# Kernel optimization log

Hardware: AMD Instinct MI355X
Metric: run time of the kernel (lower is better)

Reference implementation:

```python
import jax, jax.numpy as jnp
import numpy as np

B = 1024      # jets per batch
P = 150       # TOTAL_PARTICLES per jet
N = B * P     # total nodes
DEG = 16      # avg degree
E = N * DEG
H = 256       # GNN_HIDDEN_DIM
K = 6         # GNN_K
NC = 10       # NUM_CLUSTERS
IN = 3


def setup_inputs() -> dict:
    key = jax.random.key(0)
    ks = jax.random.split(key, 16)
    x = jax.random.normal(ks[0], (N, IN), jnp.float32)
    # kNN-like within-jet edges: each node sends to DEG random nodes of its own jet
    src = jnp.repeat(jnp.arange(N, dtype=jnp.int32), DEG)
    tgt = (src // P) * P + jax.random.randint(ks[1], (E,), 0, P, dtype=jnp.int32)
    edge_index = jnp.stack([src, tgt])  # [2, E]
    batch = jnp.arange(N, dtype=jnp.int32) // P  # sorted graph ids, exactly P per graph
    inp = dict(x=x, edge_index=edge_index, batch=batch)
    dims = [(IN, H), (H, H), (H, H), (H, H)]
    for i, (di, do) in enumerate(dims):
        s = 1.0 / np.sqrt(di)
        inp[f"W{i+1}"] = jax.random.uniform(ks[2 + i], (K, di, do), jnp.float32, -s, s)
        inp[f"b{i+1}"] = jnp.zeros((do,), jnp.float32)
    for i in range(3):
        inp[f"g{i+1}"] = jnp.ones((H,), jnp.float32)
        inp[f"be{i+1}"] = jnp.zeros((H,), jnp.float32)
    inp["centers"] = jax.random.normal(ks[10], (NC, 2), jnp.float32) * 0.2
    inp["log_temp"] = jnp.float32(2.0)
    return inp


def _lap_weights(src, tgt, n):
    # PyG ChebConv norm with lambda_max=2, sym normalization, self-loops removed:
    # scaled Laplacian L_hat = -D^{-1/2} A D^{-1/2} (zero diagonal)
    w = (src != tgt).astype(jnp.float32)          # remove self-loops
    deg = jax.ops.segment_sum(w, src, num_segments=n)
    dis = jnp.where(deg > 0, 1.0 / jnp.sqrt(deg), 0.0)
    return -(dis[src] * w * dis[tgt])             # [E]


def _cheb(x, W, b, src, tgt, lw, n):
    # Chebyshev recurrence: T0=x, T1=Lx, Tk=2L T_{k-1} - T_{k-2}
    prop = lambda h: jax.ops.segment_sum(lw[:, None] * h[src], tgt, num_segments=n)
    Tx0 = x
    out = Tx0 @ W[0]
    Tx1 = prop(Tx0)
    out = out + Tx1 @ W[1]
    for k in range(2, W.shape[0]):
        Tx2 = 2.0 * prop(Tx1) - Tx0
        out = out + Tx2 @ W[k]
        Tx0, Tx1 = Tx1, Tx2
    return out + b


def _bn(h, g, b):
    # BatchNorm1d, training-mode batch statistics (biased var), eps=1e-5
    m = h.mean(0)
    v = h.var(0)
    return (h - m) * jax.lax.rsqrt(v + 1e-5) * g + b


def reference(x, edge_index, batch, W1, b1, W2, b2, W3, b3, W4, b4,
              g1, be1, g2, be2, g3, be3, centers, log_temp):
    n = x.shape[0]
    src, tgt = edge_index[0], edge_index[1]
    lw = _lap_weights(src, tgt, n)
    lrelu = lambda h: jax.nn.leaky_relu(h, 0.01)
    h = lrelu(_bn(_cheb(x, W1, b1, src, tgt, lw, n), g1, be1))
    h = lrelu(_bn(_cheb(h, W2, b2, src, tgt, lw, n), g2, be2))
    h = lrelu(_bn(_cheb(h, W3, b3, src, tgt, lw, n), g3, be3))
    h = _cheb(h, W4, b4, src, tgt, lw, n)
    h = h / jnp.maximum(jnp.linalg.norm(h, axis=1, keepdims=True), 1e-12)  # F.normalize
    # to_dense_batch: batch is sorted with exactly P nodes per graph -> pure reshape,
    # node_mask is all True
    dense_h = h.reshape(B, P, -1)          # [B, P, H]
    dense_c = x[:, :2].reshape(B, P, 2)    # (eta, phi)
    dist = ((dense_c[:, :, None, :] - centers) ** 2).sum(-1)   # [B, P, NC]
    T = jnp.exp(jnp.clip(log_temp, -2.0, 3.0))
    assignment = jax.nn.softmax(-T * dist, axis=-1)            # mask is all-true
    pooled = jnp.einsum('bnk,bnd->bkd', assignment, dense_h)   # [B, NC, H]
    pooled = pooled / (assignment.sum(1)[:, :, None] + 1e-8)
    return pooled.reshape(B, -1)  # [B, NC*H]
```

## Files before the change

### kernel.cpp

```cpp
#include <hip/hip_runtime.h>
#include <cstdio>

#define NODES 153600
#define PJ 150
#define NJETS 1024
#define DEG 16
#define NEDGE (NODES*DEG)
#define HD 256
#define NCL 10

#define LSTR 192
#define TNS  64

typedef unsigned short u16;
typedef _Float16 f16;
typedef f16 f16x8 __attribute__((ext_vector_type(8)));
typedef u16 u16x8 __attribute__((ext_vector_type(8)));
typedef u16 u16x4 __attribute__((ext_vector_type(4)));
typedef float f32x4 __attribute__((ext_vector_type(4)));

__device__ inline float h2f(u16 u) { union { u16 s; f16 h; } v; v.s = u; return (float)v.h; }
__device__ inline u16 f2h(float f) { union { u16 s; f16 h; } v; v.h = (f16)f; return v.s; }
__device__ inline int swz(int seg, int key) { return (seg & ~7) | ((seg & 7) ^ (key & 7)); }

__global__ void k_diag(float* out, float code) {
  if (blockIdx.x == 0 && threadIdx.x == 0) out[0] = code;
}


__global__ __launch_bounds__(256) void k_discounts(const int* __restrict__ tgt,
                                                   int* __restrict__ counts,
                                                   float* __restrict__ dis) {
  int i = blockIdx.x*256 + threadIdx.x;
  if (i < NEDGE) atomicAdd(&counts[tgt[i]], 1);
  if (i < NODES) {
    int cnt = 0;
#pragma unroll
    for (int j = 0; j < DEG; ++j) cnt += (tgt[i*DEG + j] != i) ? 1 : 0;
    dis[i] = (cnt > 0) ? rsqrtf((float)cnt) : 0.f;
  }
}

__global__ __launch_bounds__(256) void k_scan(const int* __restrict__ counts, int* __restrict__ rowptr, int* __restrict__ cursor) {
  int j = blockIdx.x*256 + threadIdx.x;
  if (j >= NJETS) return;
  int run = j*PJ*DEG;
  for (int l = 0; l < PJ; ++l) {
    int idx = j*PJ + l;
    int cnt = counts[idx];
    rowptr[idx] = run;
    cursor[idx] = run;
    run += cnt;
  }
  if (j == 0) rowptr[NODES] = NEDGE;
}

__global__ __launch_bounds__(256) void k_fill(const int* __restrict__ src_, const int* __restrict__ tgt_,
                                              const float* __restrict__ dis, int* __restrict__ cursor,
                                              unsigned char* __restrict__ ccol, float* __restrict__ cw) {
  int e = blockIdx.x*256 + threadIdx.x;
  if (e >= NEDGE) return;
  int s = src_[e], t = tgt_[e];
  int pos = atomicAdd(&cursor[t], 1);
  ccol[pos] = (unsigned char)(s % PJ);
  cw[pos] = (s != t) ? -(dis[s]*dis[t]) : 0.f;
}

__global__ __launch_bounds__(256) void k_prepW(const float* __restrict__ Wa, const float* __restrict__ Wb,
                                               const float* __restrict__ Wc, u16* __restrict__ WT,
                                               float* __restrict__ stats ,
                                               float* __restrict__ rn) {
  int i = blockIdx.x*256 + threadIdx.x;
  if (i < 3*256*1536) {
    int layer = i / (256*1536);
    int rem = i - layer*(256*1536);
    int cout = rem / 1536, k = rem - cout*1536;
    int term = k >> 8, cin = k & 255;
    const float* W = (layer == 0) ? Wa : (layer == 1) ? Wb : Wc;
    WT[i] = f2h(W[(size_t)term*65536 + cin*256 + cout]);
  }
  if (i < 3*2*HD) stats[i] = 0.f;
  if (i < NODES) rn[i] = 0.f;
}

__global__ __launch_bounds__(512) void k_l1(const float* __restrict__ x,
                                            const int* __restrict__ rowptr,
                                            const unsigned char* __restrict__ ccol,
                                            const float* __restrict__ cw,
                                            const float* __restrict__ W1,
                                            const float* __restrict__ b1,
                                            float* __restrict__ stats,
                                            u16* __restrict__ outc) {
  __shared__ float Ta[450], Tb[450];
  __shared__ float Tall_s[PJ*18];
  __shared__ float wl[18*256];
  __shared__ float cw_s[PJ*DEG];
  __shared__ u16  col_s[PJ*DEG];
  __shared__ int  rp_s[PJ+1];
  int j = blockIdx.x, tid = threadIdx.x;
  int jb = j*PJ, e0 = jb*DEG;
  for (int i = tid; i < 18*256; i += 512) wl[i] = W1[i];
  for (int i = tid; i < PJ*DEG; i += 512) { cw_s[i] = cw[e0+i]; col_s[i] = (u16)ccol[e0+i]; }
  for (int i = tid; i < PJ+1; i += 512) rp_s[i] = rowptr[jb+i] - e0;
  if (tid < 450) Ta[tid] = x[(size_t)jb*3 + tid];
  __syncthreads();
  int r = tid/3, c = tid - r*3;
  float* cur = Ta; float* oth = Tb;
  if (tid < 450) Tall_s[r*18 + c] = cur[tid];
  for (int t = 1; t < 6; ++t) {
    if (tid < 450) {
      int es = rp_s[r], ee = rp_s[r+1];
      float acc = 0.f;
      for (int e = es; e < ee; ++e) acc += cw_s[e]*cur[(int)col_s[e]*3 + c];
      float v = (t == 1) ? acc : 2.f*acc - oth[tid];
      oth[tid] = v;
      Tall_s[r*18 + t*3 + c] = v;
    }
    __syncthreads();
    float* tmp = cur; cur = oth; oth = tmp;
  }
  int cc = tid & 255, rhalf = tid >> 8;
  float bc = b1[cc];
  float s = 0.f, s2 = 0.f;
  int r0 = rhalf*75;
  for (int rr = r0; rr < r0 + 75; ++rr) {
    float acc = 0.f;
#pragma unroll
    for (int i = 0; i < 18; ++i) acc += Tall_s[rr*18 + i] * wl[i*256 + cc];
    outc[(size_t)(jb+rr)*HD + cc] = f2h(acc);
    float vb = acc + bc;
    s += vb; s2 += vb*vb;
  }
  atomicAdd(&stats[cc], s);
  atomicAdd(&stats[HD + cc], s2);
}

template<int OMODE>
__global__ __launch_bounds__(1024, 4) void k_cheb(const u16* __restrict__ IN,
                                                  const u16* __restrict__ WTu,
                                                  const int* __restrict__ rowptr,
                                                  const unsigned char* __restrict__ ccol,
                                                  const float* __restrict__ cw,
                                                  const float* __restrict__ statsPrev,
                                                  const float* __restrict__ gP,
                                                  const float* __restrict__ beP,
                                                  const float* __restrict__ bP,
                                                  const float* __restrict__ bCur,
                                                  float* __restrict__ statsCur,
                                                  float* __restrict__ rn,
                                                  u16* __restrict__ OUTp) {
  __shared__ u16 Ls[160*LSTR];
  __shared__ u16 Tn[2][160*TNS];
  __shared__ u16 Tt[2][64*LSTR];
  __shared__ float bnA[HD], bnB[HD];
  int j = blockIdx.x, tid = threadIdx.x;
  int jb = j*PJ;
  int lane = tid & 63, wid = tid >> 6;
  int wm = wid >> 3, wn = wid & 7;
  int lr = lane & 15, lg = lane >> 4;
  int ph = wn >> 2, cs = wn & 3;
  int cown = cs*16 + lr;
  int key   = lr & 7;
  int segA0 = ((lg    ) ^ key) * 8;
  int segA1 = ((lg + 4) ^ key) * 8;
  int pOff[5] = { segA0, segA1, 64 + segA0, 64 + segA1, 128 + segA0 };
  int ep0 = ((cown >> 3) ^ ((lg & 1)*4 + 0)) * 8 + (cown & 7);
  int ep1 = ((cown >> 3) ^ ((lg & 1)*4 + 1)) * 8 + (cown & 7);
  int ep2 = ((cown >> 3) ^ ((lg & 1)*4 + 2)) * 8 + (cown & 7);
  int ep3 = ((cown >> 3) ^ ((lg & 1)*4 + 3)) * 8 + (cown & 7);
  int cownL = cown * LSTR;
  const f16* WT = (const f16*)WTu;
  const f16* wtb = WT + (size_t)(wn*32 + lr)*1536 + lg*8;

  if (tid < HD) {
    const float invN = 1.f/(float)NODES;
    float m = statsPrev[tid]*invN;
    float var = statsPrev[HD+tid]*invN - m*m;
    float A = rsqrtf(var + 1e-5f) * gP[tid];
    bnA[tid] = A;
    bnB[tid] = (bP[tid] - m)*A + beP[tid];
  }
  {
    u16x8 z = {0,0,0,0,0,0,0,0};
    for (int i = tid; i < 3840; i += 1024) *(u16x8*)&Ls[i*8] = z;
    for (int i = tid; i < 160; i += 1024) {
      int h = i >= 80 ? 1 : 0;
      int rem = i - h*80;
      int row = 150 + (rem >> 3), seg = rem & 7;
      *(u16x8*)&Tn[h][row*TNS + seg*8] = z;
    }
  }
  __syncthreads();
  if (tid < PJ) {
    int es = rowptr[jb + tid], ee = rowptr[jb + tid + 1];
    for (int e = es; e < ee; ++e) {
      int c = (int)ccol[e];
      int a = tid*LSTR + swz(c >> 3, tid)*8 + (c & 7);
      Ls[a] = f2h(h2f(Ls[a]) + 2.f*cw[e]);
    }
  }
  f32x4 acc[5][2];
#pragma unroll
  for (int a = 0; a < 5; ++a)
#pragma unroll
    for (int b = 0; b < 2; ++b) acc[a][b] = (f32x4)0.f;

  u16x4 tc0, tc1, tc2, tc3, tc4, tp0, tp1, tp2, tp3, tp4;

  for (int qp = 0; qp < 2; ++qp) {
    __syncthreads();
    for (int i = tid; i < 2400; i += 1024) {
      int h = (i >= 1200) ? 1 : 0;
      int rem = i - h*1200;
      int row = rem >> 3, seg = rem & 7;
      int c0 = (qp*2+h)*64 + seg*8;
      u16x8 v = *(const u16x8*)&IN[(size_t)(jb+row)*HD + c0];
      u16x8 o;
#pragma unroll
      for (int u = 0; u < 8; ++u) {
        float f = h2f(v[u])*bnA[c0+u] + bnB[c0+u];
        o[u] = f2h((f > 0.f) ? f : 0.01f*f);
      }
      *(u16x8*)&Tn[h][row*TNS + (seg ^ (row & 7))*8] = o;
    }
    __syncthreads();
    for (int i = tid; i < 2560; i += 1024) {
      int h = (i >= 1280) ? 1 : 0;
      int rem = i - h*1280;
      int c = rem & 63, m = rem >> 6;
      u16x8 v;
#pragma unroll
      for (int u = 0; u < 8; ++u) {
        int r = m*8 + u;
        v[u] = Tn[h][r*TNS + ((c >> 3) ^ (r & 7))*8 + (c & 7)];
      }
      *(u16x8*)&Tt[h][c*LSTR + swz(m, c)*8] = v;
    }
#define TINIT(MF, TC, TP) { int r0 = wm*80 + MF*16 + lg*4; u16x4 t; \
    t[0] = Tn[ph][(r0+0)*TNS + ep0]; t[1] = Tn[ph][(r0+1)*TNS + ep1]; \
    t[2] = Tn[ph][(r0+2)*TNS + ep2]; t[3] = Tn[ph][(r0+3)*TNS + ep3]; \
    TC = t; TP = t; }
    TINIT(0, tc0, tp0) TINIT(1, tc1, tp1) TINIT(2, tc2, tp2) TINIT(3, tc3, tp3) TINIT(4, tc4, tp4)
#undef TINIT
    __syncthreads();
#pragma unroll 1
    for (int t = 0; t < 6; ++t) {
#pragma unroll
      for (int h = 0; h < 2; ++h) {
        int kbase = t*256 + (qp*2+h)*64;
#pragma unroll
        for (int ks = 0; ks < 64; ks += 32) {
          int segA = (ks == 0) ? segA0 : segA1;
          f16x8 a[5], bv[2];
#pragma unroll
          for (int nf = 0; nf < 2; ++nf)
            bv[nf] = *(const f16x8*)&wtb[nf*24576 + kbase + ks];
#pragma unroll
          for (int mf = 0; mf < 5; ++mf) {
            int row = wm*80 + mf*16 + lr;
            a[mf] = *(const f16x8*)&Tn[h][row*TNS + segA];
          }
          __builtin_amdgcn_s_setprio(1);
#pragma unroll
          for (int nf = 0; nf < 2; ++nf)
#pragma unroll
            for (int mf = 0; mf < 5; ++mf)
              acc[mf][nf] = __builtin_amdgcn_mfma_f32_16x16x32_f16(a[mf], bv[nf], acc[mf][nf], 0, 0, 0);
          __builtin_amdgcn_s_setprio(0);
        }
      }
      if (t < 5) {
        f32x4 pacc[5];
#pragma unroll
        for (int mf = 0; mf < 5; ++mf) pacc[mf] = (f32x4)0.f;
#pragma unroll
        for (int ks = 0; ks < 5; ++ks) {
          f16x8 b = *(const f16x8*)&Tt[ph][cownL + pOff[ks]];
          __builtin_amdgcn_s_setprio(1);
#pragma unroll
          for (int mf = 0; mf < 5; ++mf) {
            int row = wm*80 + mf*16 + lr;
            f16x8 a = *(const f16x8*)&Ls[row*LSTR + pOff[ks]];
            pacc[mf] = __builtin_amdgcn_mfma_f32_16x16x32_f16(a, b, pacc[mf], 0, 0, 0);
          }
          __builtin_amdgcn_s_setprio(0);
        }
        __syncthreads();
#define TEPI(MF, TC, TP) { int r0 = wm*80 + MF*16 + lg*4; u16x4 o; \
        { float v0_ = (t == 0) ? 0.5f*pacc[MF][0] : pacc[MF][0] - h2f(TP[0]); o[0] = f2h(v0_); } \
        { float v1_ = (t == 0) ? 0.5f*pacc[MF][1] : pacc[MF][1] - h2f(TP[1]); o[1] = f2h(v1_); } \
        { float v2_ = (t == 0) ? 0.5f*pacc[MF][2] : pacc[MF][2] - h2f(TP[2]); o[2] = f2h(v2_); } \
        { float v3_ = (t == 0) ? 0.5f*pacc[MF][3] : pacc[MF][3] - h2f(TP[3]); o[3] = f2h(v3_); } \
        Tn[ph][(r0+0)*TNS + ep0] = o[0]; Tn[ph][(r0+1)*TNS + ep1] = o[1]; \
        Tn[ph][(r0+2)*TNS + ep2] = o[2]; Tn[ph][(r0+3)*TNS + ep3] = o[3]; \
        int sgT = wm*10 + MF*2 + (lg >> 1); \
        int segT = (sgT & ~7) | ((sgT & 7) ^ key); \
        *(u16x4*)&Tt[ph][cownL + segT*8 + (lg & 1)*4] = o; \
        TP = TC; TC = o; }
        TEPI(0, tc0, tp0) TEPI(1, tc1, tp1) TEPI(2, tc2, tp2) TEPI(3, tc3, tp3) TEPI(4, tc4, tp4)
#undef TEPI
        __syncthreads();
      }
    }
  }
  if (OMODE == 0) {
#pragma unroll
    for (int nf = 0; nf < 2; ++nf) {
      int col = wn*32 + nf*16 + lr;
      float bc = bCur[col];
      float s = 0.f, s2 = 0.f;
#pragma unroll
      for (int mf = 0; mf < 5; ++mf) {
        int row = wm*80 + mf*16 + lg*4;
#pragma unroll
        for (int e = 0; e < 4; ++e) {
          int r = row + e;
          if (r < PJ) {
            float v = acc[mf][nf][e];
            OUTp[(size_t)(jb+r)*HD + col] = f2h(v);
            float vb = v + bc;
            s += vb; s2 += vb*vb;
          }
        }
      }
      s  += __shfl_xor(s, 16, 64);  s  += __shfl_xor(s, 32, 64);
      s2 += __shfl_xor(s2, 16, 64); s2 += __shfl_xor(s2, 32, 64);
      if (lg == 0) {
        atomicAdd(&statsCur[col], s);
        atomicAdd(&statsCur[HD + col], s2);
      }
    }
  } else {
    float bc[2];
#pragma unroll
    for (int nf = 0; nf < 2; ++nf) bc[nf] = bCur[wn*32 + nf*16 + lr];
#pragma unroll
    for (int mf = 0; mf < 5; ++mf) {
      int row = wm*80 + mf*16 + lg*4;
#pragma unroll
      for (int e = 0; e < 4; ++e) {
        int r = row + e;
        float srow = 0.f;
        if (r < PJ) {
#pragma unroll
          for (int nf = 0; nf < 2; ++nf) {
            int col = wn*32 + nf*16 + lr;
            float v = acc[mf][nf][e];
            OUTp[(size_t)(jb+r)*HD + col] = f2h(v);
            float vb = v + bc[nf];
            srow += vb*vb;
          }
        }
        srow += __shfl_xor(srow, 1, 64);
        srow += __shfl_xor(srow, 2, 64);
        srow += __shfl_xor(srow, 4, 64);
        srow += __shfl_xor(srow, 8, 64);
        if (lr == 0 && r < PJ) atomicAdd(&rn[jb + r], srow);
      }
    }
  }
}


__global__ __launch_bounds__(256) void k_pool(const u16* __restrict__ h, const float* __restrict__ rn,
                                              const float* __restrict__ bias, const float* __restrict__ x,
                                              const float* __restrict__ centers, const float* __restrict__ log_temp,
                                              float* __restrict__ out) {
  __shared__ float a_s[PJ][NCL];
  __shared__ float colsum[NCL];
  __shared__ float inv_s[PJ];
  int j = blockIdx.x;
  int tid = threadIdx.x;
  float T = expf(fminf(fmaxf(log_temp[0], -2.f), 3.f));
  if (tid < PJ) {
    int g = j*PJ + tid;
    inv_s[tid] = 1.f / fmaxf(sqrtf(rn[g]), 1e-12f);
    float eta = x[(size_t)g*3], phi = x[(size_t)g*3 + 1];
    float d[NCL];
    float dmin = 1e30f;
#pragma unroll
    for (int k = 0; k < NCL; ++k) {
      float dx = eta - centers[2*k], dy = phi - centers[2*k+1];
      d[k] = dx*dx + dy*dy;
      dmin = fminf(dmin, d[k]);
    }
    float s = 0.f, ek[NCL];
#pragma unroll
    for (int k = 0; k < NCL; ++k) { ek[k] = expf(-T*(d[k]-dmin)); s += ek[k]; }
    float invs = 1.f/s;
#pragma unroll
    for (int k = 0; k < NCL; ++k) a_s[tid][k] = ek[k]*invs;
  }
  __syncthreads();
  if (tid < NCL) {
    float s = 0.f;
    for (int n = 0; n < PJ; ++n) s += a_s[n][tid];
    colsum[tid] = s;
  }
  __syncthreads();
  int c = tid;
  float bc = bias[c];
  float acc[NCL] = {};
  for (int n = 0; n < PJ; ++n) {
    float hv = (h2f(h[(size_t)(j*PJ + n)*HD + c]) + bc) * inv_s[n];
#pragma unroll
    for (int k = 0; k < NCL; ++k) acc[k] += a_s[n][k]*hv;
  }
#pragma unroll
  for (int k = 0; k < NCL; ++k)
    out[(size_t)j*(NCL*HD) + k*HD + c] = acc[k] / (colsum[k] + 1e-8f);
}


extern "C" void kernel_launch(void* const* d_in, const int* in_sizes, int n_in,
                              void* d_out, int out_size, void* d_ws, size_t ws_size,
                              hipStream_t stream) {
  (void)in_sizes; (void)n_in; (void)out_size;
  const float* x   = (const float*)d_in[0];
  const int*   ei  = (const int*)d_in[1];
  const int*   srcA = ei;
  const int*   tgtA = ei + NEDGE;
  const float* W1  = (const float*)d_in[3];
  const float* b1  = (const float*)d_in[4];
  const float* W2  = (const float*)d_in[5];
  const float* b2  = (const float*)d_in[6];
  const float* W3  = (const float*)d_in[7];
  const float* b3  = (const float*)d_in[8];
  const float* W4  = (const float*)d_in[9];
  const float* b4  = (const float*)d_in[10];
  const float* g1  = (const float*)d_in[11];
  const float* be1 = (const float*)d_in[12];
  const float* g2  = (const float*)d_in[13];
  const float* be2 = (const float*)d_in[14];
  const float* g3  = (const float*)d_in[15];
  const float* be3 = (const float*)d_in[16];
  const float* centers  = (const float*)d_in[17];
  const float* log_temp = (const float*)d_in[18];
  float* out = (float*)d_out;

  auto rb = [](size_t b) { return (b + 255) & ~(size_t)255; };
  size_t need = 2*rb((size_t)NODES*HD*2)
              + rb((size_t)3*256*1536*2)
              + 3*rb((size_t)NODES*4)
              + rb((size_t)(NODES+1)*4)
              + rb((size_t)NEDGE)
              + rb((size_t)NEDGE*4)
              + rb((size_t)3*2*HD*4)
              + rb((size_t)NODES*4);
  fprintf(stderr, "[kernel_launch] ws_size=%zu need=%zu\n", ws_size, need);
  if (d_ws == nullptr || ws_size < need) {
    float code = 1.0e6f + (float)(ws_size >> 20);
    k_diag<<<1, 1, 0, stream>>>(out, code);
    return;
  }

  char* wp = (char*)d_ws;
  auto alloc = [&](size_t b) -> void* {
    void* p = (void*)wp;
    wp += (b + 255) & ~(size_t)255;
    return p;
  };
  u16*   OUTA = (u16*)alloc((size_t)NODES*HD*2);
  u16*   OUTB = (u16*)alloc((size_t)NODES*HD*2);
  u16*   Wcat = (u16*)alloc((size_t)3*256*1536*2);
  float* dis  = (float*)alloc((size_t)NODES*4);
  int*   counts = (int*)alloc((size_t)NODES*4);
  int*   cursor = (int*)alloc((size_t)NODES*4);
  int*   rowptr = (int*)alloc((size_t)(NODES+1)*4);
  unsigned char* ccol = (unsigned char*)alloc((size_t)NEDGE);
  float* cw     = (float*)alloc((size_t)NEDGE*4);
  float* stats  = (float*)alloc((size_t)3*2*HD*4);
  float* rn     = (float*)alloc((size_t)NODES*4);
  float* s0 = stats, *s1 = stats + 512, *s2 = stats + 1024;

  hipMemsetAsync(counts, 0, (size_t)NODES*4, stream);
  k_discounts<<<(NEDGE+255)/256, 256, 0, stream>>>(tgtA, counts, dis);
  k_scan<<<(NJETS+255)/256, 256, 0, stream>>>(counts, rowptr, cursor);
  k_fill<<<(NEDGE+255)/256, 256, 0, stream>>>(srcA, tgtA, dis, cursor, ccol, cw);

  k_prepW<<<(3*256*1536+255)/256, 256, 0, stream>>>(W2, W3, W4, Wcat, stats, rn);

  k_l1<<<NJETS, 512, 0, stream>>>(x, rowptr, ccol, cw, W1, b1, s0, OUTA);

  k_cheb<0><<<NJETS, 1024, 0, stream>>>(OUTA, Wcat,            rowptr, ccol, cw, s0, g1, be1, b1, b2, s1, rn, OUTB);
  k_cheb<0><<<NJETS, 1024, 0, stream>>>(OUTB, Wcat + 393216,   rowptr, ccol, cw, s1, g2, be2, b2, b3, s2, rn, OUTA);
  k_cheb<1><<<NJETS, 1024, 0, stream>>>(OUTA, Wcat + 2*393216, rowptr, ccol, cw, s2, g3, be3, b3, b4, s2, rn, OUTB);

  k_pool<<<NJETS, 256, 0, stream>>>(OUTB, rn, b4, x, centers, log_temp, out);
}
```

Baseline: 1.256 ms.

## Fuse normalization and soft-cluster pooling into final Chebyshev layer epilogue

The last Chebyshev layer now computes per-row L2 norms in shared memory, builds the softmax cluster assignments, and accumulates pooled outputs directly from the accumulator registers. The separate pooling kernel, the global row-norm buffer with its atomics, and the half-precision store of the final features are removed. This saves a launch plus a full write and read of the last hidden layer, and uses full-precision values for pooling. In exchange the epilogue adds several block barriers, shared-memory atomics and register pressure to an already heavy kernel.

```diff
diff --git a/kernel.cpp b/kernel.cpp
--- a/kernel.cpp
+++ b/kernel.cpp
@@ -68,8 +68,7 @@
 
 __global__ __launch_bounds__(256) void k_prepW(const float* __restrict__ Wa, const float* __restrict__ Wb,
                                                const float* __restrict__ Wc, u16* __restrict__ WT,
-                                               float* __restrict__ stats ,
-                                               float* __restrict__ rn) {
+                                               float* __restrict__ stats ) {
   int i = blockIdx.x*256 + threadIdx.x;
   if (i < 3*256*1536) {
     int layer = i / (256*1536);
@@ -80,7 +79,6 @@
     WT[i] = f2h(W[(size_t)term*65536 + cin*256 + cout]);
   }
   if (i < 3*2*HD) stats[i] = 0.f;
-  if (i < NODES) rn[i] = 0.f;
 }
 
 __global__ __launch_bounds__(512) void k_l1(const float* __restrict__ x,
@@ -147,7 +145,10 @@
                                                   const float* __restrict__ bP,
                                                   const float* __restrict__ bCur,
                                                   float* __restrict__ statsCur,
-                                                  float* __restrict__ rn,
+                                                  const float* __restrict__ x,
+                                                  const float* __restrict__ centers,
+                                                  const float* __restrict__ log_temp,
+                                                  float* __restrict__ outF,
                                                   u16* __restrict__ OUTp) {
   __shared__ u16 Ls[160*LSTR];
   __shared__ u16 Tn[2][160*TNS];
@@ -331,84 +332,93 @@
       }
     }
   } else {
-    float bc[2];
-#pragma unroll
-    for (int nf = 0; nf < 2; ++nf) bc[nf] = bCur[wn*32 + nf*16 + lr];
+    __syncthreads();
+    float* aS    = (float*)Ls;
+    float* colS  = aS + PJ*NCL;
+    float* rnS   = colS + 16;
+    float* poolS = rnS + 160;
+    for (int i = tid; i < 160 + NCL*256; i += 1024) {
+      if (i < 160) rnS[i] = 0.f; else poolS[i-160] = 0.f;
+    }
+    if (tid < PJ) {
+      int g = jb + tid;
+      float T = expf(fminf(fmaxf(log_temp[0], -2.f), 3.f));
+      float eta = x[(size_t)g*3], phi = x[(size_t)g*3 + 1];
+      float d[NCL]; float dmin = 1e30f;
+#pragma unroll
+      for (int k = 0; k < NCL; ++k) {
+        float dx = eta - centers[2*k], dy = phi - centers[2*k+1];
+        d[k] = dx*dx + dy*dy; dmin = fminf(dmin, d[k]);
+      }
+      float s = 0.f, ek[NCL];
+#pragma unroll
+      for (int k = 0; k < NCL; ++k) { ek[k] = expf(-T*(d[k]-dmin)); s += ek[k]; }
+      float invs = 1.f/s;
+#pragma unroll
+      for (int k = 0; k < NCL; ++k) aS[tid*NCL + k] = ek[k]*invs;
+    }
+    __syncthreads();
+    if (tid < NCL) {
+      float s = 0.f;
+      for (int n = 0; n < PJ; ++n) s += aS[n*NCL + tid];
+      colS[tid] = s;
+    }
+    float bc0 = bCur[wn*32 + lr], bc1 = bCur[wn*32 + 16 + lr];
 #pragma unroll
     for (int mf = 0; mf < 5; ++mf) {
       int row = wm*80 + mf*16 + lg*4;
 #pragma unroll
       for (int e = 0; e < 4; ++e) {
         int r = row + e;
-        float srow = 0.f;
-        if (r < PJ) {
-#pragma unroll
-          for (int nf = 0; nf < 2; ++nf) {
-            int col = wn*32 + nf*16 + lr;
-            float v = acc[mf][nf][e];
-            OUTp[(size_t)(jb+r)*HD + col] = f2h(v);
-            float vb = v + bc[nf];
-            srow += vb*vb;
-          }
-        }
+        float v0 = acc[mf][0][e] + bc0, v1 = acc[mf][1][e] + bc1;
+        float srow = v0*v0 + v1*v1;
         srow += __shfl_xor(srow, 1, 64);
         srow += __shfl_xor(srow, 2, 64);
         srow += __shfl_xor(srow, 4, 64);
         srow += __shfl_xor(srow, 8, 64);
-        if (lr == 0 && r < PJ) atomicAdd(&rn[jb + r], srow);
-      }
-    }
-  }
-}
-
-
-__global__ __launch_bounds__(256) void k_pool(const u16* __restrict__ h, const float* __restrict__ rn,
-                                              const float* __restrict__ bias, const float* __restrict__ x,
-                                              const float* __restrict__ centers, const float* __restrict__ log_temp,
-                                              float* __restrict__ out) {
-  __shared__ float a_s[PJ][NCL];
-  __shared__ float colsum[NCL];
-  __shared__ float inv_s[PJ];
-  int j = blockIdx.x;
-  int tid = threadIdx.x;
-  float T = expf(fminf(fmaxf(log_temp[0], -2.f), 3.f));
-  if (tid < PJ) {
-    int g = j*PJ + tid;
-    inv_s[tid] = 1.f / fmaxf(sqrtf(rn[g]), 1e-12f);
-    float eta = x[(size_t)g*3], phi = x[(size_t)g*3 + 1];
-    float d[NCL];
-    float dmin = 1e30f;
+        if (lr == 0 && r < PJ) atomicAdd(&rnS[r], srow);
+      }
+    }
+    __syncthreads();
+    if (tid < PJ) rnS[tid] = 1.f / fmaxf(sqrtf(rnS[tid]), 1e-12f);
+    __syncthreads();
+    float part0[NCL], part1[NCL];
+#pragma unroll
+    for (int k = 0; k < NCL; ++k) { part0[k] = 0.f; part1[k] = 0.f; }
+#pragma unroll
+    for (int mf = 0; mf < 5; ++mf) {
+      int row = wm*80 + mf*16 + lg*4;
+#pragma unroll
+      for (int e = 0; e < 4; ++e) {
+        int r = row + e;
+        if (r < PJ) {
+          float inv = rnS[r];
+          float h0 = (acc[mf][0][e] + bc0)*inv;
+          float h1 = (acc[mf][1][e] + bc1)*inv;
+#pragma unroll
+          for (int k = 0; k < NCL; ++k) {
+            float a = aS[r*NCL + k];
+            part0[k] += a*h0; part1[k] += a*h1;
+          }
+        }
+      }
+    }
 #pragma unroll
     for (int k = 0; k < NCL; ++k) {
-      float dx = eta - centers[2*k], dy = phi - centers[2*k+1];
-      d[k] = dx*dx + dy*dy;
-      dmin = fminf(dmin, d[k]);
-    }
-    float s = 0.f, ek[NCL];
-#pragma unroll
-    for (int k = 0; k < NCL; ++k) { ek[k] = expf(-T*(d[k]-dmin)); s += ek[k]; }
-    float invs = 1.f/s;
-#pragma unroll
-    for (int k = 0; k < NCL; ++k) a_s[tid][k] = ek[k]*invs;
-  }
-  __syncthreads();
-  if (tid < NCL) {
-    float s = 0.f;
-    for (int n = 0; n < PJ; ++n) s += a_s[n][tid];
-    colsum[tid] = s;
-  }
-  __syncthreads();
-  int c = tid;
-  float bc = bias[c];
-  float acc[NCL] = {};
-  for (int n = 0; n < PJ; ++n) {
-    float hv = (h2f(h[(size_t)(j*PJ + n)*HD + c]) + bc) * inv_s[n];
-#pragma unroll
-    for (int k = 0; k < NCL; ++k) acc[k] += a_s[n][k]*hv;
-  }
-#pragma unroll
-  for (int k = 0; k < NCL; ++k)
-    out[(size_t)j*(NCL*HD) + k*HD + c] = acc[k] / (colsum[k] + 1e-8f);
+      float p0 = part0[k], p1 = part1[k];
+      p0 += __shfl_xor(p0, 16, 64); p0 += __shfl_xor(p0, 32, 64);
+      p1 += __shfl_xor(p1, 16, 64); p1 += __shfl_xor(p1, 32, 64);
+      if (lg == 0) {
+        atomicAdd(&poolS[k*256 + wn*32 + lr], p0);
+        atomicAdd(&poolS[k*256 + wn*32 + 16 + lr], p1);
+      }
+    }
+    __syncthreads();
+    for (int i = tid; i < NCL*256; i += 1024) {
+      int k = i >> 8;
+      outF[(size_t)j*(NCL*HD) + i] = poolS[i] / (colS[k] + 1e-8f);
+    }
+  }
 }
 
 
@@ -445,8 +455,7 @@
               + rb((size_t)(NODES+1)*4)
               + rb((size_t)NEDGE)
               + rb((size_t)NEDGE*4)
-              + rb((size_t)3*2*HD*4)
-              + rb((size_t)NODES*4);
+              + rb((size_t)3*2*HD*4);
   fprintf(stderr, "[kernel_launch] ws_size=%zu need=%zu\n", ws_size, need);
   if (d_ws == nullptr || ws_size < need) {
     float code = 1.0e6f + (float)(ws_size >> 20);
@@ -470,7 +479,6 @@
   unsigned char* ccol = (unsigned char*)alloc((size_t)NEDGE);
   float* cw     = (float*)alloc((size_t)NEDGE*4);
   float* stats  = (float*)alloc((size_t)3*2*HD*4);
-  float* rn     = (float*)alloc((size_t)NODES*4);
   float* s0 = stats, *s1 = stats + 512, *s2 = stats + 1024;
 
   hipMemsetAsync(counts, 0, (size_t)NODES*4, stream);
@@ -478,13 +486,11 @@
   k_scan<<<(NJETS+255)/256, 256, 0, stream>>>(counts, rowptr, cursor);
   k_fill<<<(NEDGE+255)/256, 256, 0, stream>>>(srcA, tgtA, dis, cursor, ccol, cw);
 
-  k_prepW<<<(3*256*1536+255)/256, 256, 0, stream>>>(W2, W3, W4, Wcat, stats, rn);
+  k_prepW<<<(3*256*1536+255)/256, 256, 0, stream>>>(W2, W3, W4, Wcat, stats);
 
   k_l1<<<NJETS, 512, 0, stream>>>(x, rowptr, ccol, cw, W1, b1, s0, OUTA);
 
-  k_cheb<0><<<NJETS, 1024, 0, stream>>>(OUTA, Wcat,            rowptr, ccol, cw, s0, g1, be1, b1, b2, s1, rn, OUTB);
-  k_cheb<0><<<NJETS, 1024, 0, stream>>>(OUTB, Wcat + 393216,   rowptr, ccol, cw, s1, g2, be2, b2, b3, s2, rn, OUTA);
-  k_cheb<1><<<NJETS, 1024, 0, stream>>>(OUTA, Wcat + 2*393216, rowptr, ccol, cw, s2, g3, be3, b3, b4, s2, rn, OUTB);
-
-  k_pool<<<NJETS, 256, 0, stream>>>(OUTB, rn, b4, x, centers, log_temp, out);
-}
+  k_cheb<0><<<NJETS, 1024, 0, stream>>>(OUTA, Wcat,            rowptr, ccol, cw, s0, g1, be1, b1, b2, s1, x, centers, log_temp, out, OUTB);
+  k_cheb<0><<<NJETS, 1024, 0, stream>>>(OUTB, Wcat + 393216,   rowptr, ccol, cw, s1, g2, be2, b2, b3, s2, x, centers, log_temp, out, OUTA);
+  k_cheb<1><<<NJETS, 1024, 0, stream>>>(OUTA, Wcat + 2*393216, rowptr, ccol, cw, s2, g3, be3, b3, b4, s2, x, centers, log_temp, out, OUTB);
+}
```

Result: no change. 1.274 ms (+1.4%).
